# Performance work log

Hardware: AMD Instinct MI355X
Metric: run time of the kernel (lower is better)

## Reference

```python
import jax, jax.numpy as jnp
import numpy as np

B, C, NA = 32, 9, 65440
GAMMA = 3.0
SCALE_XY = 1.0 / 0.1
SCALE_WH = 1.0 / 0.2


def setup_inputs() -> dict:
    key = jax.random.key(0)
    k1, k2, k3, k4, k5 = jax.random.split(key, 5)
    bbox_delta = jax.random.normal(k1, (B, 4, NA), dtype=jnp.float32)
    confs = jax.random.normal(k2, (B, C, NA), dtype=jnp.float32)
    # gt boxes in xywh, keep w/h strictly positive for the log() in _loc_vec
    gt_bbox = jax.random.uniform(k3, (B, NA, 4), dtype=jnp.float32, minval=0.05, maxval=1.0)
    gt_labels = jax.random.randint(k4, (B, NA), 0, C, dtype=jnp.int32)
    anchors = jax.random.uniform(k5, (1, 4, NA), dtype=jnp.float32, minval=0.1, maxval=1.0)
    return {"bbox_delta": bbox_delta, "confs": confs, "gt_bbox": gt_bbox,
            "gt_labels": gt_labels, "anchors": anchors}


def reference(bbox_delta, confs, gt_bbox, gt_labels, anchors):
    n_classes = confs.shape[1]
    # ---- focal classification loss (fused: no one-hot materialized) ----
    # alpha = [10, 1000, ..., 1000]; einsum 'a,bcd->bad' followed by sum(dim=1)
    # collapses to multiplying by sum(alpha) since y is one-hot over c.
    alpha = jnp.full((n_classes,), 1000.0, dtype=jnp.float32).at[0].set(10.0)
    logp = jax.nn.log_softmax(confs, axis=1)              # [B,C,N]
    t = gt_labels.astype(jnp.int32)[:, None, :]           # [B,1,N]
    logp_t = jnp.take_along_axis(logp, t, axis=1)[:, 0, :]  # [B,N]
    p_t = jnp.exp(logp_t)
    focal = (1.0 - p_t) ** GAMMA * logp_t                 # [B,N]
    classification_loss = jnp.mean(-jnp.sum(alpha) * focal)

    # ---- localization loss (masked smooth-L1, no boolean compaction) ----
    gt_t = jnp.transpose(gt_bbox, (0, 2, 1))               # [B,4,N]
    gxy = SCALE_XY * (gt_t[:, :2, :] - anchors[:, :2, :]) / anchors[:, 2:, :]
    gwh = SCALE_WH * jnp.log(gt_t[:, 2:, :] / anchors[:, 2:, :])
    gt_loc = jnp.concatenate([gxy, gwh], axis=1)           # [B,4,N]

    pos = gt_labels > 0                                    # [B,N]
    mask = pos[:, None, :]                                 # broadcast over 4 coords
    diff = jnp.where(mask, bbox_delta - gt_loc, 0.0)
    ad = jnp.abs(diff)
    sl1 = jnp.where(ad < 1.0, 0.5 * diff * diff, ad - 0.5)
    regression_loss = jnp.sum(jnp.where(mask, sl1, 0.0))
    num_pos = jnp.sum(pos).astype(jnp.float32)

    total_loss = regression_loss / num_pos + classification_loss
    return total_loss
```

## Files before the change

### kernel.cpp

```cpp
#include <hip/hip_runtime.h>
#include <math.h>

constexpr int B  = 32;
constexpr int C  = 9;
constexpr int NA = 65440;
constexpr int PER_B    = NA / 4;
constexpr int NTHREADS = B * PER_B;
constexpr int BLOCK    = 256;
constexpr int GRID     = NTHREADS / BLOCK;

constexpr int WS_REG = 2048;
constexpr int WS_POS = 4096;

__device__ __forceinline__ float4 ld4(const float* p) {
    return *reinterpret_cast<const float4*>(p);
}

__device__ __forceinline__ float smooth_l1(float d) {
    float ad = fabsf(d);
    return ad < 1.0f ? 0.5f * d * d : ad - 0.5f;
}

__global__ __launch_bounds__(BLOCK, 4) void ssd_main(
    const float* __restrict__ bbox_delta,
    const float* __restrict__ confs,
    const float* __restrict__ gt_bbox,
    const int*   __restrict__ gt_labels,
    const float* __restrict__ anchors,
    float* __restrict__ ws)
{
    const int tid = blockIdx.x * BLOCK + threadIdx.x;
    const int b   = tid / PER_B;
    const int a   = (tid - b * PER_B) * 4;

    const float* cbase = confs + (size_t)b * C * NA + a;
    float4 cf0 = ld4(cbase);
    float4 cf1 = ld4(cbase + 1 * NA);
    float4 cf2 = ld4(cbase + 2 * NA);
    float4 cf3 = ld4(cbase + 3 * NA);
    float4 cf4 = ld4(cbase + 4 * NA);
    float4 cf5 = ld4(cbase + 5 * NA);
    float4 cf6 = ld4(cbase + 6 * NA);
    float4 cf7 = ld4(cbase + 7 * NA);
    float4 cf8 = ld4(cbase + 8 * NA);

    const int4 lab = *reinterpret_cast<const int4*>(gt_labels + (size_t)b * NA + a);

    const float* abase = anchors + a;
    float4 ax = ld4(abase);
    float4 ay = ld4(abase + NA);
    float4 aw = ld4(abase + 2 * NA);
    float4 ah = ld4(abase + 3 * NA);

    const float* dbase = bbox_delta + (size_t)b * 4 * NA + a;
    float4 d0 = ld4(dbase);
    float4 d1 = ld4(dbase + NA);
    float4 d2 = ld4(dbase + 2 * NA);
    float4 d3 = ld4(dbase + 3 * NA);

    const float* gbase = gt_bbox + ((size_t)b * NA + a) * 4;
    float4 g0 = ld4(gbase);
    float4 g1 = ld4(gbase + 4);
    float4 g2 = ld4(gbase + 8);
    float4 g3 = ld4(gbase + 12);

    float4 cf[C] = {cf0, cf1, cf2, cf3, cf4, cf5, cf6, cf7, cf8};
    float sex = 0.f, sey = 0.f, sez = 0.f, sew = 0.f;
    float ctx = cf0.x, cty = cf0.y, ctz = cf0.z, ctw = cf0.w;
#pragma unroll
    for (int c = 0; c < C; ++c) {
        sex += __expf(cf[c].x);
        sey += __expf(cf[c].y);
        sez += __expf(cf[c].z);
        sew += __expf(cf[c].w);
        ctx = (lab.x == c) ? cf[c].x : ctx;
        cty = (lab.y == c) ? cf[c].y : cty;
        ctz = (lab.z == c) ? cf[c].z : ctz;
        ctw = (lab.w == c) ? cf[c].w : ctw;
    }
    float lpx = ctx - __logf(sex);
    float lpy = cty - __logf(sey);
    float lpz = ctz - __logf(sez);
    float lpw = ctw - __logf(sew);

    float focal;
    {
        float px = __expf(lpx), py = __expf(lpy), pz = __expf(lpz), pw = __expf(lpw);
        float ox = 1.f - px, oy = 1.f - py, oz = 1.f - pz, ow = 1.f - pw;
        focal = ox*ox*ox*lpx + oy*oy*oy*lpy + oz*oz*oz*lpz + ow*ow*ow*lpw;
    }

    float reg = 0.f, pcnt = 0.f;
#define DO_ANCHOR(GT, AXC, AYC, AWC, AHC, D0C, D1C, D2C, D3C, LABC)               \
    {                                                                             \
        float gx = 10.0f * __fdividef(GT.x - AXC, AWC);                           \
        float gy = 10.0f * __fdividef(GT.y - AYC, AHC);                           \
        float gw = 5.0f * __logf(__fdividef(GT.z, AWC));                          \
        float gh = 5.0f * __logf(__fdividef(GT.w, AHC));                          \
        float s  = smooth_l1(D0C - gx) + smooth_l1(D1C - gy) +                    \
                   smooth_l1(D2C - gw) + smooth_l1(D3C - gh);                     \
        if (LABC > 0) { reg += s; pcnt += 1.0f; }                                 \
    }
    DO_ANCHOR(g0, ax.x, ay.x, aw.x, ah.x, d0.x, d1.x, d2.x, d3.x, lab.x)
    DO_ANCHOR(g1, ax.y, ay.y, aw.y, ah.y, d0.y, d1.y, d2.y, d3.y, lab.y)
    DO_ANCHOR(g2, ax.z, ay.z, aw.z, ah.z, d0.z, d1.z, d2.z, d3.z, lab.z)
    DO_ANCHOR(g3, ax.w, ay.w, aw.w, ah.w, d0.w, d1.w, d2.w, d3.w, lab.w)
#undef DO_ANCHOR

#pragma unroll
    for (int off = 32; off > 0; off >>= 1) {
        focal += __shfl_down(focal, off, 64);
        reg   += __shfl_down(reg,   off, 64);
        pcnt  += __shfl_down(pcnt,  off, 64);
    }
    __shared__ float sf[4], sr[4], sp[4];
    const int wid  = threadIdx.x >> 6;
    const int lane = threadIdx.x & 63;
    if (lane == 0) { sf[wid] = focal; sr[wid] = reg; sp[wid] = pcnt; }
    __syncthreads();
    if (threadIdx.x == 0) {
        ws[blockIdx.x]          = sf[0] + sf[1] + sf[2] + sf[3];
        ws[WS_REG + blockIdx.x] = sr[0] + sr[1] + sr[2] + sr[3];
        ws[WS_POS + blockIdx.x] = sp[0] + sp[1] + sp[2] + sp[3];
    }
}

__global__ __launch_bounds__(256) void finalize_k(const float* __restrict__ ws,
                                                  float* __restrict__ out) {
    float F = 0.f, R = 0.f, P = 0.f;
    for (int i = threadIdx.x; i < GRID; i += 256) {
        F += ws[i];
        R += ws[WS_REG + i];
        P += ws[WS_POS + i];
    }
#pragma unroll
    for (int off = 32; off > 0; off >>= 1) {
        F += __shfl_down(F, off, 64);
        R += __shfl_down(R, off, 64);
        P += __shfl_down(P, off, 64);
    }
    __shared__ float sf[4], sr[4], sp[4];
    const int wid  = threadIdx.x >> 6;
    const int lane = threadIdx.x & 63;
    if (lane == 0) { sf[wid] = F; sr[wid] = R; sp[wid] = P; }
    __syncthreads();
    if (threadIdx.x == 0) {
        float Ft = sf[0] + sf[1] + sf[2] + sf[3];
        float Rt = sr[0] + sr[1] + sr[2] + sr[3];
        float Pt = sp[0] + sp[1] + sp[2] + sp[3];
        const float inv_n = 1.0f / (float)((size_t)B * NA);
        out[0] = Rt / Pt - 8010.0f * Ft * inv_n;
    }
}

extern "C" void kernel_launch(void* const* d_in, const int* in_sizes, int n_in,
                              void* d_out, int out_size, void* d_ws, size_t ws_size,
                              hipStream_t stream) {
    const float* bbox_delta = (const float*)d_in[0];
    const float* confs      = (const float*)d_in[1];
    const float* gt_bbox    = (const float*)d_in[2];
    const int*   gt_labels  = (const int*)d_in[3];
    const float* anchors    = (const float*)d_in[4];
    float* ws  = (float*)d_ws;
    float* out = (float*)d_out;

    ssd_main<<<GRID, BLOCK, 0, stream>>>(bbox_delta, confs, gt_bbox, gt_labels, anchors, ws);
    finalize_k<<<1, 256, 0, stream>>>(ws, out);
}
```

Before: 174.4 us.

## Process one anchor per thread with scalar coalesced loads and atomic fallback

Switches from four anchors per thread with float4 loads to one anchor per thread with scalar coalesced loads and a single float4 gt_bbox load, so the grid is four times larger. The goal is more memory-level parallelism, fewer registers per thread, and contiguous gt_bbox access across lanes. A workspace-size check now chooses between per-block partials (8192 blocks) and an atomicAdd path with extra zeroing and finalize kernels. The trade-off is four times as many blocks to reduce and narrower memory transactions.

```diff
diff --git a/kernel.cpp b/kernel.cpp
--- a/kernel.cpp
+++ b/kernel.cpp
@@ -4,23 +4,20 @@
 constexpr int B  = 32;
 constexpr int C  = 9;
 constexpr int NA = 65440;
-constexpr int PER_B    = NA / 4;
-constexpr int NTHREADS = B * PER_B;
-constexpr int BLOCK    = 256;
-constexpr int GRID     = NTHREADS / BLOCK;
+constexpr int BLOCK   = 256;
+constexpr int NTH     = B * NA;
+constexpr int GRID    = NTH / BLOCK;
 
-constexpr int WS_REG = 2048;
-constexpr int WS_POS = 4096;
-
-__device__ __forceinline__ float4 ld4(const float* p) {
-    return *reinterpret_cast<const float4*>(p);
-}
+constexpr int WS_REG = 8192;
+constexpr int WS_POS = 16384;
+constexpr size_t WS_NEEDED = (size_t)(WS_POS + 8192) * sizeof(float);
 
 __device__ __forceinline__ float smooth_l1(float d) {
     float ad = fabsf(d);
     return ad < 1.0f ? 0.5f * d * d : ad - 0.5f;
 }
 
+template <bool ATOMIC>
 __global__ __launch_bounds__(BLOCK, 4) void ssd_main(
     const float* __restrict__ bbox_delta,
     const float* __restrict__ confs,
@@ -30,82 +27,57 @@
     float* __restrict__ ws)
 {
     const int tid = blockIdx.x * BLOCK + threadIdx.x;
-    const int b   = tid / PER_B;
-    const int a   = (tid - b * PER_B) * 4;
+    const int b   = tid / NA;
+    const int a   = tid - b * NA;
 
-    const float* cbase = confs + (size_t)b * C * NA + a;
-    float4 cf0 = ld4(cbase);
-    float4 cf1 = ld4(cbase + 1 * NA);
-    float4 cf2 = ld4(cbase + 2 * NA);
-    float4 cf3 = ld4(cbase + 3 * NA);
-    float4 cf4 = ld4(cbase + 4 * NA);
-    float4 cf5 = ld4(cbase + 5 * NA);
-    float4 cf6 = ld4(cbase + 6 * NA);
-    float4 cf7 = ld4(cbase + 7 * NA);
-    float4 cf8 = ld4(cbase + 8 * NA);
+    const float* cb = confs + (size_t)b * C * NA + a;
+    float c0 = cb[0];
+    float c1 = cb[1 * NA];
+    float c2 = cb[2 * NA];
+    float c3 = cb[3 * NA];
+    float c4 = cb[4 * NA];
+    float c5 = cb[5 * NA];
+    float c6 = cb[6 * NA];
+    float c7 = cb[7 * NA];
+    float c8 = cb[8 * NA];
 
-    const int4 lab = *reinterpret_cast<const int4*>(gt_labels + (size_t)b * NA + a);
+    const int lab = gt_labels[(size_t)b * NA + a];
 
-    const float* abase = anchors + a;
-    float4 ax = ld4(abase);
-    float4 ay = ld4(abase + NA);
-    float4 aw = ld4(abase + 2 * NA);
-    float4 ah = ld4(abase + 3 * NA);
+    const float ax = anchors[a];
+    const float ay = anchors[NA + a];
+    const float aw = anchors[2 * NA + a];
+    const float ah = anchors[3 * NA + a];
 
-    const float* dbase = bbox_delta + (size_t)b * 4 * NA + a;
-    float4 d0 = ld4(dbase);
-    float4 d1 = ld4(dbase + NA);
-    float4 d2 = ld4(dbase + 2 * NA);
-    float4 d3 = ld4(dbase + 3 * NA);
+    const float* db = bbox_delta + (size_t)b * 4 * NA + a;
+    const float d0 = db[0];
+    const float d1 = db[NA];
+    const float d2 = db[2 * NA];
+    const float d3 = db[3 * NA];
 
-    const float* gbase = gt_bbox + ((size_t)b * NA + a) * 4;
-    float4 g0 = ld4(gbase);
-    float4 g1 = ld4(gbase + 4);
-    float4 g2 = ld4(gbase + 8);
-    float4 g3 = ld4(gbase + 12);
+    const float4 g = *reinterpret_cast<const float4*>(gt_bbox + ((size_t)b * NA + a) * 4);
 
-    float4 cf[C] = {cf0, cf1, cf2, cf3, cf4, cf5, cf6, cf7, cf8};
-    float sex = 0.f, sey = 0.f, sez = 0.f, sew = 0.f;
-    float ctx = cf0.x, cty = cf0.y, ctz = cf0.z, ctw = cf0.w;
+    float cf[C] = {c0, c1, c2, c3, c4, c5, c6, c7, c8};
+    float se = 0.f;
+    float ct = c0;
 #pragma unroll
     for (int c = 0; c < C; ++c) {
-        sex += __expf(cf[c].x);
-        sey += __expf(cf[c].y);
-        sez += __expf(cf[c].z);
-        sew += __expf(cf[c].w);
-        ctx = (lab.x == c) ? cf[c].x : ctx;
-        cty = (lab.y == c) ? cf[c].y : cty;
-        ctz = (lab.z == c) ? cf[c].z : ctz;
-        ctw = (lab.w == c) ? cf[c].w : ctw;
+        se += __expf(cf[c]);
+        ct  = (lab == c) ? cf[c] : ct;
     }
-    float lpx = ctx - __logf(sex);
-    float lpy = cty - __logf(sey);
-    float lpz = ctz - __logf(sez);
-    float lpw = ctw - __logf(sew);
+    const float lp = ct - __logf(se);
+    const float p  = __expf(lp);
+    const float o  = 1.f - p;
+    float focal = o * o * o * lp;
 
-    float focal;
-    {
-        float px = __expf(lpx), py = __expf(lpy), pz = __expf(lpz), pw = __expf(lpw);
-        float ox = 1.f - px, oy = 1.f - py, oz = 1.f - pz, ow = 1.f - pw;
-        focal = ox*ox*ox*lpx + oy*oy*oy*lpy + oz*oz*oz*lpz + ow*ow*ow*lpw;
-    }
-
-    float reg = 0.f, pcnt = 0.f;
-#define DO_ANCHOR(GT, AXC, AYC, AWC, AHC, D0C, D1C, D2C, D3C, LABC)               \
-    {                                                                             \
-        float gx = 10.0f * __fdividef(GT.x - AXC, AWC);                           \
-        float gy = 10.0f * __fdividef(GT.y - AYC, AHC);                           \
-        float gw = 5.0f * __logf(__fdividef(GT.z, AWC));                          \
-        float gh = 5.0f * __logf(__fdividef(GT.w, AHC));                          \
-        float s  = smooth_l1(D0C - gx) + smooth_l1(D1C - gy) +                    \
-                   smooth_l1(D2C - gw) + smooth_l1(D3C - gh);                     \
-        if (LABC > 0) { reg += s; pcnt += 1.0f; }                                 \
-    }
-    DO_ANCHOR(g0, ax.x, ay.x, aw.x, ah.x, d0.x, d1.x, d2.x, d3.x, lab.x)
-    DO_ANCHOR(g1, ax.y, ay.y, aw.y, ah.y, d0.y, d1.y, d2.y, d3.y, lab.y)
-    DO_ANCHOR(g2, ax.z, ay.z, aw.z, ah.z, d0.z, d1.z, d2.z, d3.z, lab.z)
-    DO_ANCHOR(g3, ax.w, ay.w, aw.w, ah.w, d0.w, d1.w, d2.w, d3.w, lab.w)
-#undef DO_ANCHOR
+    const float gx = 10.0f * __fdividef(g.x - ax, aw);
+    const float gy = 10.0f * __fdividef(g.y - ay, ah);
+    const float gw = 5.0f * __logf(__fdividef(g.z, aw));
+    const float gh = 5.0f * __logf(__fdividef(g.w, ah));
+    const float s  = smooth_l1(d0 - gx) + smooth_l1(d1 - gy) +
+                     smooth_l1(d2 - gw) + smooth_l1(d3 - gh);
+    const float pos = (lab > 0) ? 1.0f : 0.0f;
+    float reg  = pos * s;
+    float pcnt = pos;
 
 #pragma unroll
     for (int off = 32; off > 0; off >>= 1) {
@@ -119,10 +91,29 @@
     if (lane == 0) { sf[wid] = focal; sr[wid] = reg; sp[wid] = pcnt; }
     __syncthreads();
     if (threadIdx.x == 0) {
-        ws[blockIdx.x]          = sf[0] + sf[1] + sf[2] + sf[3];
-        ws[WS_REG + blockIdx.x] = sr[0] + sr[1] + sr[2] + sr[3];
-        ws[WS_POS + blockIdx.x] = sp[0] + sp[1] + sp[2] + sp[3];
+        const float F = sf[0] + sf[1] + sf[2] + sf[3];
+        const float R = sr[0] + sr[1] + sr[2] + sr[3];
+        const float P = sp[0] + sp[1] + sp[2] + sp[3];
+        if (ATOMIC) {
+            atomicAdd(&ws[0],  F);
+            atomicAdd(&ws[32], R);
+            atomicAdd(&ws[64], P);
+        } else {
+            ws[blockIdx.x]          = F;
+            ws[WS_REG + blockIdx.x] = R;
+            ws[WS_POS + blockIdx.x] = P;
+        }
     }
+}
+
+__global__ void zero_ws_k(float* ws) {
+    int i = threadIdx.x;
+    if (i < 96) ws[i] = 0.0f;
+}
+
+__global__ void finalize_atomic_k(const float* __restrict__ ws, float* __restrict__ out) {
+    const float inv_n = 1.0f / (float)((size_t)B * NA);
+    out[0] = ws[32] / ws[64] - 8010.0f * ws[0] * inv_n;
 }
 
 __global__ __launch_bounds__(256) void finalize_k(const float* __restrict__ ws,
@@ -145,9 +136,9 @@
     if (lane == 0) { sf[wid] = F; sr[wid] = R; sp[wid] = P; }
     __syncthreads();
     if (threadIdx.x == 0) {
-        float Ft = sf[0] + sf[1] + sf[2] + sf[3];
-        float Rt = sr[0] + sr[1] + sr[2] + sr[3];
-        float Pt = sp[0] + sp[1] + sp[2] + sp[3];
+        const float Ft = sf[0] + sf[1] + sf[2] + sf[3];
+        const float Rt = sr[0] + sr[1] + sr[2] + sr[3];
+        const float Pt = sp[0] + sp[1] + sp[2] + sp[3];
         const float inv_n = 1.0f / (float)((size_t)B * NA);
         out[0] = Rt / Pt - 8010.0f * Ft * inv_n;
     }
@@ -164,6 +155,14 @@
     float* ws  = (float*)d_ws;
     float* out = (float*)d_out;
 
-    ssd_main<<<GRID, BLOCK, 0, stream>>>(bbox_delta, confs, gt_bbox, gt_labels, anchors, ws);
-    finalize_k<<<1, 256, 0, stream>>>(ws, out);
+    if (ws_size >= WS_NEEDED) {
+        ssd_main<false><<<GRID, BLOCK, 0, stream>>>(bbox_delta, confs, gt_bbox,
+                                                    gt_labels, anchors, ws);
+        finalize_k<<<1, 256, 0, stream>>>(ws, out);
+    } else {
+        zero_ws_k<<<1, 128, 0, stream>>>(ws);
+        ssd_main<true><<<GRID, BLOCK, 0, stream>>>(bbox_delta, confs, gt_bbox,
+                                                   gt_labels, anchors, ws);
+        finalize_atomic_k<<<1, 1, 0, stream>>>(ws, out);
+    }
 }
```

New measurement: 178.4 us. 1.02x slower.
